# Kernel tuning notes

Hardware: AMD Instinct MI355X
Metric: run time of the kernel (lower is better)

## Reference

```python
import jax, jax.numpy as jnp
import numpy as np

N_NODES = 100000
N_EDGES = 1600000
NUM_RELS = 8
IN_FEAT = 128
OUT_FEAT = 128


def setup_inputs() -> dict:
    key = jax.random.key(0)
    k1, k2, k3, k4, k5 = jax.random.split(key, 5)
    feat = jax.random.normal(k1, (N_NODES, IN_FEAT), dtype=jnp.float32)
    weight = jax.random.normal(k2, (NUM_RELS, IN_FEAT, OUT_FEAT), dtype=jnp.float32) * 0.05
    src = jax.random.randint(k3, (N_EDGES,), 0, N_NODES, dtype=jnp.int64 if jax.config.jax_enable_x64 else jnp.int32)
    dst = jax.random.randint(k4, (N_EDGES,), 0, N_NODES, dtype=jnp.int64 if jax.config.jax_enable_x64 else jnp.int32)
    etypes = jax.random.randint(k5, (N_EDGES,), 0, NUM_RELS, dtype=jnp.int64 if jax.config.jax_enable_x64 else jnp.int32)
    return {"feat": feat, "weight": weight, "src": src, "dst": dst, "etypes": etypes}


def reference(feat, weight, src, dst, etypes):
    # RGCN segment_mm: per edge e, message m_e = feat[src[e]] @ weight[etypes[e]],
    # then sum-aggregate messages into destination nodes.
    # The torch module sorts edges by etype only so segment_mm can run a grouped
    # GEMM; the scatter-sum aggregation is order-independent, so sorting does not
    # change the math. We compute all per-relation projections densely (small R)
    # and gather the right one per edge -- equivalent math, fully vectorized.
    proj = jnp.einsum('ni,rio->rno', feat, weight)      # [R, N, out]
    m = proj[etypes, src]                               # [E, out] gather per edge
    out = jax.ops.segment_sum(m, dst, num_segments=feat.shape[0])  # [N, out]
    return out
```

## Files before the change

### kernel.cpp

```cpp
#include <hip/hip_runtime.h>
#include <hip/hip_bf16.h>


#define FEAT 128
#define CAP 512
#define CHUNK 128

typedef __attribute__((ext_vector_type(8))) short short8;
typedef __attribute__((ext_vector_type(8))) __bf16 bf16x8;
typedef __attribute__((ext_vector_type(4))) float f32x4;
typedef __attribute__((ext_vector_type(2))) unsigned int uint2v;

__device__ __forceinline__ unsigned f2bf(float x) {
    union { float f; unsigned u; } v; v.f = x;
    unsigned r = v.u + 0x7FFFu + ((v.u >> 16) & 1u);
    return r >> 16;
}

__global__ void cvt_feat_kernel(const float* __restrict__ f,
                                ushort* __restrict__ o, int n8) {
    int i = blockIdx.x * blockDim.x + threadIdx.x;
    if (i >= n8) return;
    const float4* f4 = (const float4*)f;
    float4 a = f4[2 * i], b = f4[2 * i + 1];
    union { ushort u[8]; int4 v; } pk;
    pk.u[0] = f2bf(a.x); pk.u[1] = f2bf(a.y); pk.u[2] = f2bf(a.z); pk.u[3] = f2bf(a.w);
    pk.u[4] = f2bf(b.x); pk.u[5] = f2bf(b.y); pk.u[6] = f2bf(b.z); pk.u[7] = f2bf(b.w);
    ((int4*)o)[i] = pk.v;
}

__global__ void cvt_w_kernel(const float* __restrict__ w,
                             ushort* __restrict__ wt, int total) {
    int i = blockIdx.x * blockDim.x + threadIdx.x;
    if (i >= total) return;
    int r = i >> 14, n = (i >> 7) & 127, k = i & 127;
    wt[i] = (ushort)f2bf(w[(r << 14) + (k << 7) + n]);
}

__global__ void scatter_kernel(const int* __restrict__ dst,
                               const int* __restrict__ et,
                               const int* __restrict__ src, int E, int R,
                               int sbits, int* __restrict__ cursor,
                               int* __restrict__ recs) {
    int i = blockIdx.x * blockDim.x + threadIdx.x;
    int stride = gridDim.x * blockDim.x;
    for (; i < E; i += stride) {
        int d = dst[i];
        int b = (d >> 7) * R + et[i];
        int p = atomicAdd(&cursor[b], 1);
        if (p < CAP) recs[(size_t)b * CAP + p] = src[i] | ((d & 127) << sbits);
    }
}

__global__ __launch_bounds__(256, 2)
void fused_kernel(const ushort* __restrict__ featb,
                  const ushort* __restrict__ wtr,
                  const int* __restrict__ recs,
                  const int* __restrict__ cursor,
                  float* __restrict__ out, int N, int R, int sbits) {
    __shared__ __align__(16) ushort GS[128 * 128];
    __shared__ __align__(16) ushort Wl[128 * 128];
    __shared__ __align__(16) ushort dlv[CHUNK];

    int t = threadIdx.x;
    int qid = t >> 4, cc = t & 15;
    int lane = t & 63, wid = t >> 6;
    int lm = lane & 15, lq = lane >> 4;
    int blk = blockIdx.x, base = blk * 128;
    int er = (wid >> 1) * 64;
    int nw = (wid & 1) * 64;
    int fr = er, dc = nw;
    int smask = (1 << sbits) - 1;
    int l7 = lm & 7;

    f32x4 acc[16];
    #pragma unroll
    for (int i = 0; i < 16; i++) acc[i] = (f32x4){0.f, 0.f, 0.f, 0.f};

    for (int r = 0; r < R; r++) {
        int bkt = blk * R + r;
        int ecnt = cursor[bkt];
        if (ecnt <= 0) continue;
        if (ecnt > CAP) ecnt = CAP;
        const int* rb = recs + (size_t)bkt * CAP;

        const ushort* wsrc = wtr + ((size_t)r << 14);
        #pragma unroll
        for (int j = 0; j < 8; j++) {
            int idx = j * 2048 + t * 8;
            uint4 v = *(const uint4*)(wsrc + idx);
            int n = idx >> 7;
            *(uint4*)&Wl[(n << 7) + ((cc ^ (qid & 7)) << 3)] = v;
        }

        int dlp[8]; uint4 gvv[8];
        #pragma unroll
        for (int p = 0; p < 8; p++) {
            int j = p * 16 + qid;
            int rc = (j < ecnt) ? rb[j] : -1;
            dlp[p] = (rc >= 0) ? ((rc >> sbits) & 127) : 0xFFFF;
            if (rc >= 0)
                gvv[p] = *(const uint4*)(featb + (size_t)(rc & smask) * FEAT + cc * 8);
            else
                gvv[p] = (uint4){0u, 0u, 0u, 0u};
        }

        for (int c0 = 0; c0 < ecnt; c0 += CHUNK) {
            #pragma unroll
            for (int p = 0; p < 8; p++) {
                int row = p * 16 + qid;
                *(uint4*)&GS[(row << 7) + ((cc ^ (qid & 7)) << 3)] = gvv[p];
            }
            if (cc == 0) {
                #pragma unroll
                for (int p = 0; p < 8; p++)
                    dlv[p * 16 + qid] = (ushort)dlp[p];
            }
            __syncthreads();

            f32x4 Ta[16];
            #pragma unroll
            for (int i = 0; i < 16; i++) Ta[i] = (f32x4){0.f, 0.f, 0.f, 0.f};
            #pragma unroll
            for (int ks = 0; ks < 4; ks++) {
                int kb = ks * 4 + lq;
                int kswz = (kb ^ l7) << 3;
                short8 af[4], bw[4];
                #pragma unroll
                for (int tm = 0; tm < 4; tm++)
                    af[tm] = *(const short8*)&GS[((er + tm * 16 + lm) << 7) + kswz];
                #pragma unroll
                for (int tn = 0; tn < 4; tn++)
                    bw[tn] = *(const short8*)&Wl[((nw + tn * 16 + lm) << 7) + kswz];
                #pragma unroll
                for (int tm = 0; tm < 4; tm++)
                    #pragma unroll
                    for (int tn = 0; tn < 4; tn++)
                        Ta[tm * 4 + tn] = __builtin_amdgcn_mfma_f32_16x16x32_bf16(
                            __builtin_bit_cast(bf16x8, af[tm]),
                            __builtin_bit_cast(bf16x8, bw[tn]),
                            Ta[tm * 4 + tn], 0, 0, 0);
            }
            __syncthreads();

            int rcn[8];
            bool more = (c0 + CHUNK < ecnt);
            if (more) {
                #pragma unroll
                for (int p = 0; p < 8; p++) {
                    int j = c0 + CHUNK + p * 16 + qid;
                    rcn[p] = (j < ecnt) ? rb[j] : -1;
                }
            }

            #pragma unroll
            for (int tm = 0; tm < 4; tm++)
                #pragma unroll
                for (int tn = 0; tn < 4; tn++) {
                    f32x4 v = Ta[tm * 4 + tn];
                    union { unsigned u[2]; uint2v w; } pk;
                    pk.u[0] = f2bf(v[0]) | (f2bf(v[1]) << 16);
                    pk.u[1] = f2bf(v[2]) | (f2bf(v[3]) << 16);
                    int w = nw + tn * 16 + lm;
                    int eb = er + tm * 16 + lq * 4;
                    *(uint2v*)&GS[(w << 7) + (((eb >> 3) ^ (w & 7)) << 3) +
                                  (eb & 7)] = pk.w;
                }

            if (more) {
                #pragma unroll
                for (int p = 0; p < 8; p++) {
                    int rc = rcn[p];
                    dlp[p] = (rc >= 0) ? ((rc >> sbits) & 127) : 0xFFFF;
                    if (rc >= 0)
                        gvv[p] = *(const uint4*)(featb +
                                 (size_t)(rc & smask) * FEAT + cc * 8);
                    else
                        gvv[p] = (uint4){0u, 0u, 0u, 0u};
                }
            }

            asm volatile("s_waitcnt lgkmcnt(0)" ::: "memory");
            __builtin_amdgcn_s_barrier();
            __builtin_amdgcn_sched_barrier(0);

            #pragma unroll
            for (int ks = 0; ks < 4; ks++) {
                int kof = ks * 32 + lq * 8;
                int kb2 = ks * 4 + lq;
                union { ushort u[8]; uint4 v; } dl8;
                dl8.v = *(const uint4*)&dlv[kof];
                short8 at[4];
                #pragma unroll
                for (int tm = 0; tm < 4; tm++) {
                    int row = fr + tm * 16 + lm;
                    at[tm] = *(const short8*)&GS[(row << 7) + ((kb2 ^ l7) << 3)];
                }
                short8 pb[4];
                #pragma unroll
                for (int tn = 0; tn < 4; tn++) {
                    ushort col = (ushort)(dc + tn * 16 + lm);
                    union { ushort u[8]; short8 s; } b;
                    #pragma unroll
                    for (int q = 0; q < 8; q++)
                        b.u[q] = (dl8.u[q] == col) ? (ushort)0x3F80 : (ushort)0;
                    pb[tn] = b.s;
                }
                #pragma unroll
                for (int tm = 0; tm < 4; tm++)
                    #pragma unroll
                    for (int tn = 0; tn < 4; tn++)
                        acc[tm * 4 + tn] = __builtin_amdgcn_mfma_f32_16x16x32_bf16(
                            __builtin_bit_cast(bf16x8, at[tm]),
                            __builtin_bit_cast(bf16x8, pb[tn]),
                            acc[tm * 4 + tn], 0, 0, 0);
            }

            asm volatile("s_waitcnt lgkmcnt(0)" ::: "memory");
            __builtin_amdgcn_s_barrier();
            __builtin_amdgcn_sched_barrier(0);
        }
    }

    #pragma unroll
    for (int tn = 0; tn < 4; tn++) {
        int drow = base + dc + tn * 16 + lm;
        if (drow < N) {
            #pragma unroll
            for (int tm = 0; tm < 4; tm++) {
                f32x4 v = acc[tm * 4 + tn];
                *(f32x4*)(out + (size_t)drow * FEAT + fr + tm * 16 + lq * 4) = v;
            }
        }
    }
}

static inline size_t al256(size_t x) { return (x + 255) & ~(size_t)255; }

extern "C" void kernel_launch(void* const* d_in, const int* in_sizes, int n_in,
                              void* d_out, int out_size, void* d_ws,
                              size_t ws_size, hipStream_t stream) {
    const float* feat = (const float*)d_in[0];
    const float* weight = (const float*)d_in[1];
    const int* src = (const int*)d_in[2];
    const int* dst = (const int*)d_in[3];
    const int* et = (const int*)d_in[4];

    int nfeat = in_sizes[0];
    int N = nfeat / FEAT;
    int R = in_sizes[1] / (FEAT * FEAT);
    int E = in_sizes[2];
    int Npad = ((N + 127) / 128) * 128;
    int nblk = Npad / 128;
    int NB = nblk * R;
    float* out = (float*)d_out;

    int sbits = 1;
    while ((1 << sbits) < N) sbits++;

    char* ws = (char*)d_ws;
    size_t o = 0;
    size_t cur_o  = o; o += al256((size_t)NB * 4);
    size_t recs_o = o; o += al256((size_t)NB * CAP * 4);
    size_t wtr_o  = o; o += al256((size_t)R * FEAT * FEAT * 2);
    size_t featb_o = o;

    int* cursor = (int*)(ws + cur_o);
    int* recs   = (int*)(ws + recs_o);
    ushort* wtr   = (ushort*)(ws + wtr_o);
    ushort* featb = (ushort*)(ws + featb_o);

    hipMemsetAsync(cursor, 0, (size_t)NB * 4, stream);

    int wtotal = R * FEAT * FEAT;
    cvt_w_kernel<<<(wtotal + 255) / 256, 256, 0, stream>>>(weight, wtr, wtotal);
    int n8 = nfeat / 8;
    cvt_feat_kernel<<<(n8 + 255) / 256, 256, 0, stream>>>(feat, featb, n8);

    scatter_kernel<<<512, 256, 0, stream>>>(dst, et, src, E, R, sbits,
                                            cursor, recs);

    fused_kernel<<<nblk, 256, 0, stream>>>(featb, wtr, recs, cursor,
                                           out, N, R, sbits);
}
```

Baseline: 458.2 us.

## Aggregate features per relation before weight multiply; use 512-thread blocks

The fused kernel now reorders the math to (scatter of gathered features) @ W instead of scatter of (features @ W). For each destination block and relation it first builds a transposed feature tile, accumulates the one-hot scatter product into a per-relation 128x128 partial sum, rounds it to bf16, then multiplies once by the relation weight, which is read straight from global memory. This drops the per-chunk edge-by-weight GEMM, frees the weight LDS buffer, and doubles the block to 512 threads (8 waves). The cost is an extra bf16 rounding of the aggregated sums and a transposed LDS write pattern with 32-bit stores.

```diff
diff --git a/kernel.cpp b/kernel.cpp
--- a/kernel.cpp
+++ b/kernel.cpp
@@ -52,30 +52,29 @@
     }
 }
 
-__global__ __launch_bounds__(256, 2)
+__global__ __launch_bounds__(512, 4)
 void fused_kernel(const ushort* __restrict__ featb,
                   const ushort* __restrict__ wtr,
                   const int* __restrict__ recs,
                   const int* __restrict__ cursor,
                   float* __restrict__ out, int N, int R, int sbits) {
     __shared__ __align__(16) ushort GS[128 * 128];
-    __shared__ __align__(16) ushort Wl[128 * 128];
     __shared__ __align__(16) ushort dlv[CHUNK];
 
     int t = threadIdx.x;
-    int qid = t >> 4, cc = t & 15;
-    int lane = t & 63, wid = t >> 6;
+    int lane = t & 63;
+    int wid = t >> 6;
     int lm = lane & 15, lq = lane >> 4;
+    int wr = wid >> 2;
+    int wc = wid & 3;
+    int cc = t & 15;
+    int pr = t >> 4;
     int blk = blockIdx.x, base = blk * 128;
-    int er = (wid >> 1) * 64;
-    int nw = (wid & 1) * 64;
-    int fr = er, dc = nw;
     int smask = (1 << sbits) - 1;
-    int l7 = lm & 7;
-
-    f32x4 acc[16];
+
+    f32x4 acc[8];
     #pragma unroll
-    for (int i = 0; i < 16; i++) acc[i] = (f32x4){0.f, 0.f, 0.f, 0.f};
+    for (int i = 0; i < 8; i++) acc[i] = (f32x4){0.f, 0.f, 0.f, 0.f};
 
     for (int r = 0; r < R; r++) {
         int bkt = blk * R + r;
@@ -84,122 +83,88 @@
         if (ecnt > CAP) ecnt = CAP;
         const int* rb = recs + (size_t)bkt * CAP;
 
-        const ushort* wsrc = wtr + ((size_t)r << 14);
-        #pragma unroll
-        for (int j = 0; j < 8; j++) {
-            int idx = j * 2048 + t * 8;
-            uint4 v = *(const uint4*)(wsrc + idx);
-            int n = idx >> 7;
-            *(uint4*)&Wl[(n << 7) + ((cc ^ (qid & 7)) << 3)] = v;
-        }
-
-        int dlp[8]; uint4 gvv[8];
-        #pragma unroll
-        for (int p = 0; p < 8; p++) {
-            int j = p * 16 + qid;
-            int rc = (j < ecnt) ? rb[j] : -1;
-            dlp[p] = (rc >= 0) ? ((rc >> sbits) & 127) : 0xFFFF;
-            if (rc >= 0)
-                gvv[p] = *(const uint4*)(featb + (size_t)(rc & smask) * FEAT + cc * 8);
-            else
-                gvv[p] = (uint4){0u, 0u, 0u, 0u};
-        }
+        f32x4 accST[8];
+        #pragma unroll
+        for (int i = 0; i < 8; i++) accST[i] = (f32x4){0.f, 0.f, 0.f, 0.f};
+
+        int rca[4];
+        union { uint4 v; ushort us[8]; } ga[4];
+        #pragma unroll
+        for (int w = 0; w < 2; w++)
+            #pragma unroll
+            for (int par = 0; par < 2; par++) {
+                int s = w * 2 + par;
+                int e = 2 * (pr + 32 * w) + par;
+                int rc = (e < ecnt) ? rb[e] : -1;
+                rca[s] = rc;
+                if (rc >= 0)
+                    ga[s].v = *(const uint4*)(featb +
+                              (size_t)(rc & smask) * FEAT + cc * 8);
+                else
+                    ga[s].v = (uint4){0u, 0u, 0u, 0u};
+            }
 
         for (int c0 = 0; c0 < ecnt; c0 += CHUNK) {
             #pragma unroll
-            for (int p = 0; p < 8; p++) {
-                int row = p * 16 + qid;
-                *(uint4*)&GS[(row << 7) + ((cc ^ (qid & 7)) << 3)] = gvv[p];
+            for (int w = 0; w < 2; w++) {
+                int eb8 = (pr >> 2) + 8 * w;
+                int eo = 2 * (pr & 3);
+                #pragma unroll
+                for (int j = 0; j < 8; j++) {
+                    unsigned v = (unsigned)ga[2 * w].us[j] |
+                                 ((unsigned)ga[2 * w + 1].us[j] << 16);
+                    int f = cc * 8 + j;
+                    *(unsigned*)&GS[f * 128 + ((eb8 ^ cc) << 3) + eo] = v;
+                }
             }
             if (cc == 0) {
                 #pragma unroll
-                for (int p = 0; p < 8; p++)
-                    dlv[p * 16 + qid] = (ushort)dlp[p];
+                for (int w = 0; w < 2; w++)
+                    #pragma unroll
+                    for (int par = 0; par < 2; par++) {
+                        int s = w * 2 + par;
+                        int e = 2 * (pr + 32 * w) + par;
+                        dlv[e] = (rca[s] >= 0)
+                            ? (ushort)((rca[s] >> sbits) & 127) : (ushort)0xFF;
+                    }
             }
             __syncthreads();
 
-            f32x4 Ta[16];
-            #pragma unroll
-            for (int i = 0; i < 16; i++) Ta[i] = (f32x4){0.f, 0.f, 0.f, 0.f};
+            bool more = (c0 + CHUNK) < ecnt;
+            int rcn[4];
+            union { uint4 v; ushort us[8]; } gan[4];
+            if (more) {
+                #pragma unroll
+                for (int w = 0; w < 2; w++)
+                    #pragma unroll
+                    for (int par = 0; par < 2; par++) {
+                        int s = w * 2 + par;
+                        int j = c0 + CHUNK + 2 * (pr + 32 * w) + par;
+                        int rc = (j < ecnt) ? rb[j] : -1;
+                        rcn[s] = rc;
+                        if (rc >= 0)
+                            gan[s].v = *(const uint4*)(featb +
+                                       (size_t)(rc & smask) * FEAT + cc * 8);
+                        else
+                            gan[s].v = (uint4){0u, 0u, 0u, 0u};
+                    }
+            }
+
             #pragma unroll
             for (int ks = 0; ks < 4; ks++) {
-                int kb = ks * 4 + lq;
-                int kswz = (kb ^ l7) << 3;
-                short8 af[4], bw[4];
-                #pragma unroll
-                for (int tm = 0; tm < 4; tm++)
-                    af[tm] = *(const short8*)&GS[((er + tm * 16 + lm) << 7) + kswz];
-                #pragma unroll
-                for (int tn = 0; tn < 4; tn++)
-                    bw[tn] = *(const short8*)&Wl[((nw + tn * 16 + lm) << 7) + kswz];
-                #pragma unroll
-                for (int tm = 0; tm < 4; tm++)
-                    #pragma unroll
-                    for (int tn = 0; tn < 4; tn++)
-                        Ta[tm * 4 + tn] = __builtin_amdgcn_mfma_f32_16x16x32_bf16(
-                            __builtin_bit_cast(bf16x8, af[tm]),
-                            __builtin_bit_cast(bf16x8, bw[tn]),
-                            Ta[tm * 4 + tn], 0, 0, 0);
-            }
-            __syncthreads();
-
-            int rcn[8];
-            bool more = (c0 + CHUNK < ecnt);
-            if (more) {
-                #pragma unroll
-                for (int p = 0; p < 8; p++) {
-                    int j = c0 + CHUNK + p * 16 + qid;
-                    rcn[p] = (j < ecnt) ? rb[j] : -1;
+                union { ushort u[8]; uint4 v; } dl8;
+                dl8.v = *(const uint4*)&dlv[ks * 32 + lq * 8];
+                short8 af[4];
+                #pragma unroll
+                for (int tm = 0; tm < 4; tm++) {
+                    int f = wr * 64 + tm * 16 + lm;
+                    af[tm] = *(const short8*)&GS[f * 128 +
+                             (((ks * 4 + lq) ^ (f >> 3)) << 3)];
                 }
-            }
-
-            #pragma unroll
-            for (int tm = 0; tm < 4; tm++)
-                #pragma unroll
-                for (int tn = 0; tn < 4; tn++) {
-                    f32x4 v = Ta[tm * 4 + tn];
-                    union { unsigned u[2]; uint2v w; } pk;
-                    pk.u[0] = f2bf(v[0]) | (f2bf(v[1]) << 16);
-                    pk.u[1] = f2bf(v[2]) | (f2bf(v[3]) << 16);
-                    int w = nw + tn * 16 + lm;
-                    int eb = er + tm * 16 + lq * 4;
-                    *(uint2v*)&GS[(w << 7) + (((eb >> 3) ^ (w & 7)) << 3) +
-                                  (eb & 7)] = pk.w;
-                }
-
-            if (more) {
-                #pragma unroll
-                for (int p = 0; p < 8; p++) {
-                    int rc = rcn[p];
-                    dlp[p] = (rc >= 0) ? ((rc >> sbits) & 127) : 0xFFFF;
-                    if (rc >= 0)
-                        gvv[p] = *(const uint4*)(featb +
-                                 (size_t)(rc & smask) * FEAT + cc * 8);
-                    else
-                        gvv[p] = (uint4){0u, 0u, 0u, 0u};
-                }
-            }
-
-            asm volatile("s_waitcnt lgkmcnt(0)" ::: "memory");
-            __builtin_amdgcn_s_barrier();
-            __builtin_amdgcn_sched_barrier(0);
-
-            #pragma unroll
-            for (int ks = 0; ks < 4; ks++) {
-                int kof = ks * 32 + lq * 8;
-                int kb2 = ks * 4 + lq;
-                union { ushort u[8]; uint4 v; } dl8;
-                dl8.v = *(const uint4*)&dlv[kof];
-                short8 at[4];
-                #pragma unroll
-                for (int tm = 0; tm < 4; tm++) {
-                    int row = fr + tm * 16 + lm;
-                    at[tm] = *(const short8*)&GS[(row << 7) + ((kb2 ^ l7) << 3)];
-                }
-                short8 pb[4];
-                #pragma unroll
-                for (int tn = 0; tn < 4; tn++) {
-                    ushort col = (ushort)(dc + tn * 16 + lm);
+                short8 pb[2];
+                #pragma unroll
+                for (int tn = 0; tn < 2; tn++) {
+                    ushort col = (ushort)(wc * 32 + tn * 16 + lm);
                     union { ushort u[8]; short8 s; } b;
                     #pragma unroll
                     for (int q = 0; q < 8; q++)
@@ -209,27 +174,70 @@
                 #pragma unroll
                 for (int tm = 0; tm < 4; tm++)
                     #pragma unroll
-                    for (int tn = 0; tn < 4; tn++)
-                        acc[tm * 4 + tn] = __builtin_amdgcn_mfma_f32_16x16x32_bf16(
-                            __builtin_bit_cast(bf16x8, at[tm]),
+                    for (int tn = 0; tn < 2; tn++)
+                        accST[tm * 2 + tn] = __builtin_amdgcn_mfma_f32_16x16x32_bf16(
+                            __builtin_bit_cast(bf16x8, af[tm]),
                             __builtin_bit_cast(bf16x8, pb[tn]),
-                            acc[tm * 4 + tn], 0, 0, 0);
-            }
-
-            asm volatile("s_waitcnt lgkmcnt(0)" ::: "memory");
-            __builtin_amdgcn_s_barrier();
-            __builtin_amdgcn_sched_barrier(0);
+                            accST[tm * 2 + tn], 0, 0, 0);
+            }
+            __syncthreads();
+
+            if (more) {
+                #pragma unroll
+                for (int s = 0; s < 4; s++) { rca[s] = rcn[s]; ga[s].v = gan[s].v; }
+            }
         }
+
+        #pragma unroll
+        for (int tm = 0; tm < 4; tm++)
+            #pragma unroll
+            for (int tn = 0; tn < 2; tn++) {
+                f32x4 v = accST[tm * 2 + tn];
+                union { unsigned u[2]; uint2v w; } pk;
+                pk.u[0] = f2bf(v[0]) | (f2bf(v[1]) << 16);
+                pk.u[1] = f2bf(v[2]) | (f2bf(v[3]) << 16);
+                int dst = wc * 32 + tn * 16 + lm;
+                int f4 = wr * 64 + tm * 16 + lq * 4;
+                *(uint2v*)&GS[dst * 128 + (((f4 >> 3) ^ (dst & 15)) << 3) +
+                              (f4 & 7)] = pk.w;
+            }
+        __syncthreads();
+
+        const ushort* wp = wtr + ((size_t)r << 14);
+        #pragma unroll
+        for (int ks = 0; ks < 4; ks++) {
+            short8 aw[4], bs[2];
+            #pragma unroll
+            for (int tm = 0; tm < 4; tm++) {
+                int of = wr * 64 + tm * 16 + lm;
+                aw[tm] = *(const short8*)(wp + of * 128 + ks * 32 + lq * 8);
+            }
+            #pragma unroll
+            for (int tn = 0; tn < 2; tn++) {
+                int dst = wc * 32 + tn * 16 + lm;
+                bs[tn] = *(const short8*)&GS[dst * 128 +
+                         (((ks * 4 + lq) ^ (dst & 15)) << 3)];
+            }
+            #pragma unroll
+            for (int tm = 0; tm < 4; tm++)
+                #pragma unroll
+                for (int tn = 0; tn < 2; tn++)
+                    acc[tm * 2 + tn] = __builtin_amdgcn_mfma_f32_16x16x32_bf16(
+                        __builtin_bit_cast(bf16x8, aw[tm]),
+                        __builtin_bit_cast(bf16x8, bs[tn]),
+                        acc[tm * 2 + tn], 0, 0, 0);
+        }
+        __syncthreads();
     }
 
     #pragma unroll
-    for (int tn = 0; tn < 4; tn++) {
-        int drow = base + dc + tn * 16 + lm;
+    for (int tn = 0; tn < 2; tn++) {
+        int drow = base + wc * 32 + tn * 16 + lm;
         if (drow < N) {
             #pragma unroll
             for (int tm = 0; tm < 4; tm++) {
-                f32x4 v = acc[tm * 4 + tn];
-                *(f32x4*)(out + (size_t)drow * FEAT + fr + tm * 16 + lq * 4) = v;
+                f32x4 v = acc[tm * 2 + tn];
+                *(f32x4*)(out + (size_t)drow * FEAT + wr * 64 + tm * 16 + lq * 4) = v;
             }
         }
     }
@@ -280,6 +288,6 @@
     scatter_kernel<<<512, 256, 0, stream>>>(dst, et, src, E, R, sbits,
                                             cursor, recs);
 
-    fused_kernel<<<nblk, 256, 0, stream>>>(featb, wtr, recs, cursor,
+    fused_kernel<<<nblk, 512, 0, stream>>>(featb, wtr, recs, cursor,
                                            out, N, R, sbits);
 }
```

Result: slower. 771.0 us (+68.3%).
